# Optimization experiments

Measured on AMD Instinct MI355X. Metric: run time of the kernel, lower is better.

The kernel has to match this reference:

```python
import jax, jax.numpy as jnp
import numpy as np

N_NODES = 50000
N_EDGES = 400000
N_GRAPHS = 128
D_IN = 768
D_HID = 256
D_OUT = 256
EPS_COS = 1e-8
EPS_BN = 1e-5
NEG_SLOPE = 0.2  # PyG GATConv default


def setup_inputs() -> dict:
    key = jax.random.key(0)
    ks = jax.random.split(key, 16)
    inp = {
        "claim_emb": jax.random.normal(ks[0], (N_GRAPHS, D_IN), dtype=jnp.float32),
        "x": jax.random.normal(ks[1], (N_NODES, D_IN), dtype=jnp.float32),
        "edge_index": jax.random.randint(ks[2], (2, N_EDGES), 0, N_NODES, dtype=jnp.int64 if jax.config.jax_enable_x64 else jnp.int32),
        "node_batch": jnp.sort(jax.random.randint(ks[3], (N_NODES,), 0, N_GRAPHS, dtype=jnp.int64 if jax.config.jax_enable_x64 else jnp.int32)),
        # GAT layer 1 (768 -> 256, single head)
        "W1": jax.random.normal(ks[4], (D_IN, D_HID), dtype=jnp.float32) * (1.0 / np.sqrt(D_IN)),
        "a_src1": jax.random.normal(ks[5], (D_HID,), dtype=jnp.float32) * 0.1,
        "a_dst1": jax.random.normal(ks[6], (D_HID,), dtype=jnp.float32) * 0.1,
        "b1": jnp.zeros((D_HID,), dtype=jnp.float32),
        # GAT layer 2 (256 -> 256)
        "W2": jax.random.normal(ks[7], (D_HID, D_OUT), dtype=jnp.float32) * (1.0 / np.sqrt(D_HID)),
        "a_src2": jax.random.normal(ks[8], (D_OUT,), dtype=jnp.float32) * 0.1,
        "a_dst2": jax.random.normal(ks[9], (D_OUT,), dtype=jnp.float32) * 0.1,
        "b2": jnp.zeros((D_OUT,), dtype=jnp.float32),
        # BatchNorm after layer 1
        "bn_gamma": jnp.ones((D_HID,), dtype=jnp.float32),
        "bn_beta": jnp.zeros((D_HID,), dtype=jnp.float32),
        # classifier: (gnn_out + claim_dim) -> 1
        "clf_W": jax.random.normal(ks[10], (D_OUT + D_IN, 1), dtype=jnp.float32) * (1.0 / np.sqrt(D_OUT + D_IN)),
        "clf_b": jnp.zeros((1,), dtype=jnp.float32),
    }
    return inp


def _gat_conv(x, src, dst, n_nodes, W, a_src, a_dst, b):
    """PyG GATConv, heads=1, concat=True, self-loops already appended to src/dst."""
    h = x @ W                                  # [N, H]
    alpha_s = h @ a_src                        # [N]
    alpha_d = h @ a_dst                        # [N]
    e = jax.nn.leaky_relu(alpha_s[src] + alpha_d[dst], NEG_SLOPE)  # [E]
    # segment softmax over edges grouped by destination node
    m = jax.ops.segment_max(e, dst, num_segments=n_nodes)          # [N]
    ex = jnp.exp(e - m[dst])
    denom = jax.ops.segment_sum(ex, dst, num_segments=n_nodes)     # [N]
    attn = ex / denom[dst]                                         # [E]
    out = jax.ops.segment_sum(h[src] * attn[:, None], dst, num_segments=n_nodes)
    return out + b


def reference(claim_emb, x, edge_index, node_batch,
              W1, a_src1, a_dst1, b1, W2, a_src2, a_dst2, b2,
              bn_gamma, bn_beta, clf_W, clf_b):
    n_nodes = x.shape[0]
    n_graphs = claim_emb.shape[0]

    # relevance weighting: cosine similarity between claim (per node's graph) and node feature
    ce = claim_emb[node_batch]                                      # [N, 768]
    dot = jnp.sum(ce * x, axis=-1)
    norm = jnp.linalg.norm(ce, axis=-1) * jnp.linalg.norm(x, axis=-1)
    rel = dot / jnp.maximum(norm, EPS_COS)                          # [N]
    h = x * rel[:, None]

    # add self loops (PyG GATConv default)
    loops = jnp.arange(n_nodes, dtype=edge_index.dtype)
    src = jnp.concatenate([edge_index[0], loops])
    dst = jnp.concatenate([edge_index[1], loops])

    # layer 1: GAT -> BatchNorm (training-mode batch stats) -> ReLU
    h = _gat_conv(h, src, dst, n_nodes, W1, a_src1, a_dst1, b1)
    mu = jnp.mean(h, axis=0)
    var = jnp.var(h, axis=0)
    h = (h - mu) / jnp.sqrt(var + EPS_BN) * bn_gamma + bn_beta
    h = jax.nn.relu(h)

    # layer 2: GAT -> ReLU
    h = _gat_conv(h, src, dst, n_nodes, W2, a_src2, a_dst2, b2)
    h = jax.nn.relu(h)

    # global mean pool per graph
    sums = jax.ops.segment_sum(h, node_batch, num_segments=n_graphs)            # [B, 256]
    counts = jax.ops.segment_sum(jnp.ones((n_nodes,), h.dtype), node_batch, num_segments=n_graphs)
    pooled = sums / jnp.maximum(counts, 1.0)[:, None]

    combined = jnp.concatenate([pooled, claim_emb], axis=1)                     # [B, 256+768]
    out = combined @ clf_W + clf_b                                              # [B, 1]
    return out[:, 0]
```

## Files before the change

### kernel.cpp

```cpp
#include <hip/hip_runtime.h>
#include <hip/hip_bf16.h>

#define N_NODES  50000
#define N_EDGES  400000
#define E_TOT    450000
#define N_GRAPHS 128
#define D_IN     768
#define D_HID    256

typedef __hip_bfloat16 bf16;
typedef __attribute__((ext_vector_type(8))) short short8;
typedef __attribute__((ext_vector_type(4))) short short4v;
typedef __attribute__((ext_vector_type(4))) float f32x4;

__device__ __forceinline__ float b2f(bf16 v) { return __bfloat162float(v); }
__device__ __forceinline__ float us2f(unsigned short u) { return __uint_as_float((unsigned)u << 16); }
__device__ __forceinline__ int clampN(int v) { return min(max(v, 0), N_NODES - 1); }
__device__ __forceinline__ short f2bs(float f) {
  unsigned u = __float_as_uint(f);
  return (short)((u + 0x7FFFu + ((u >> 16) & 1u)) >> 16);
}

__device__ __forceinline__ void gload_lds16(const void* g, void* l) {
  __builtin_amdgcn_global_load_lds(
      (const __attribute__((address_space(1))) void*)g,
      (__attribute__((address_space(3))) void*)l, 16, 0, 0);
}

__device__ __forceinline__ float waveReduceSum(float v) {
#pragma unroll
  for (int o = 32; o > 0; o >>= 1) v += __shfl_down(v, o);
  return v;
}

__device__ __forceinline__ float blockReduce256(float v, volatile float* buf4) {
  int lane = threadIdx.x & 63, wid = threadIdx.x >> 6;
  v = waveReduceSum(v);
  if (lane == 0) buf4[wid] = v;
  __syncthreads();
  float s = buf4[0] + buf4[1] + buf4[2] + buf4[3];
  __syncthreads();
  return s;
}

__global__ __launch_bounds__(256) void detect_idx_kernel(
    const int* __restrict__ edge32, int* __restrict__ flagNZ) {
  if (threadIdx.x == 0) *flagNZ = 0;
  __syncthreads();
  int t = threadIdx.x;
  int nz = 0;
#pragma unroll
  for (int i = 0; i < 4; ++i) {
    int idx = 2 * (t + i * 256) + 1;
    if (edge32[idx] != 0) nz = 1;
  }
  if (nz) atomicOr(flagNZ, 1);
}

__global__ __launch_bounds__(256) void normalize_idx_kernel(
    const void* __restrict__ edge, const void* __restrict__ nbin,
    const int* __restrict__ flagNZ,
    int* __restrict__ src32, int* __restrict__ dst32, int* __restrict__ nb32,
    int* __restrict__ deg,
    const float* __restrict__ W1, const float* __restrict__ W2,
    short* __restrict__ W1T, short* __restrict__ W2T) {
  bool is64 = (*flagNZ == 0);
  long i = (long)blockIdx.x * 256 + threadIdx.x;
  const int*       e32 = (const int*)edge;
  const long long* e64 = (const long long*)edge;
  const int*       n32 = (const int*)nbin;
  const long long* n64 = (const long long*)nbin;
  if (i < N_NODES) deg[i] = 0;
  if (i < N_EDGES) {
    src32[i] = clampN(is64 ? (int)e64[i] : e32[i]);
    dst32[i] = clampN(is64 ? (int)e64[N_EDGES + i] : e32[N_EDGES + i]);
  }
  long j = i - N_EDGES;
  if (j >= 0 && j < N_NODES)
    nb32[j] = min(max(is64 ? (int)n64[j] : n32[j], 0), N_GRAPHS - 1);
  int t = (int)i;
  if (t < D_IN * D_HID) {
    int n = t / D_IN, k = t - n * D_IN;
    W1T[t] = f2bs(W1[(size_t)k * D_HID + n]);
  }
  int j2 = t - D_IN * D_HID;
  if (j2 >= 0 && j2 < D_HID * D_HID) {
    int n = j2 / D_HID, k = j2 - n * D_HID;
    W2T[j2] = f2bs(W2[(size_t)k * D_HID + n]);
  }
}

__global__ __launch_bounds__(256) void hist_kernel(
    const int* __restrict__ dst, int* __restrict__ deg) {
  int i = blockIdx.x * 256 + threadIdx.x;
  if (i >= E_TOT) return;
  int d = (i < N_EDGES) ? dst[i] : (i - N_EDGES);
  atomicAdd(&deg[d], 1);
}

#define SCAN_VPT 4
#define SCAN_BLK (256 * SCAN_VPT)
#define SCAN_NB  ((N_NODES + SCAN_BLK - 1) / SCAN_BLK)

__global__ __launch_bounds__(256) void scan_local_kernel(
    const int* __restrict__ deg, int* __restrict__ incl, int* __restrict__ blockSums) {
  __shared__ int wsum[4];
  int lane = threadIdx.x & 63, wid = threadIdx.x >> 6;
  int tbase = blockIdx.x * SCAN_BLK + threadIdx.x * SCAN_VPT;
  int v[SCAN_VPT];
  int s = 0;
#pragma unroll
  for (int j = 0; j < SCAN_VPT; ++j) {
    int i = tbase + j;
    v[j] = (i < N_NODES) ? deg[i] : 0;
    s += v[j];
  }
  int sc = s;
#pragma unroll
  for (int o = 1; o < 64; o <<= 1) {
    int t = __shfl_up(sc, o);
    if (lane >= o) sc += t;
  }
  if (lane == 63) wsum[wid] = sc;
  __syncthreads();
  int woff = 0;
  for (int w = 0; w < wid; ++w) woff += wsum[w];
  int run = woff + sc - s;
#pragma unroll
  for (int j = 0; j < SCAN_VPT; ++j) {
    run += v[j];
    int i = tbase + j;
    if (i < N_NODES) incl[i] = run;
  }
  if (threadIdx.x == 255)
    blockSums[blockIdx.x] = woff + sc;
}

__global__ __launch_bounds__(256) void scan_add_kernel(
    const int* __restrict__ deg, const int* __restrict__ incl,
    const int* __restrict__ bsums,
    int* __restrict__ rowptr, int* __restrict__ pos) {
  __shared__ int offSh;
  int sb = blockIdx.x >> 2;
  if (threadIdx.x < 64) {
    int v = (threadIdx.x < sb) ? bsums[threadIdx.x] : 0;
#pragma unroll
    for (int o = 32; o > 0; o >>= 1) v += __shfl_down(v, o);
    if (threadIdx.x == 0) offSh = v;
  }
  __syncthreads();
  int i = blockIdx.x * 256 + threadIdx.x;
  if (i >= N_NODES) return;
  int ic = incl[i] + offSh;
  rowptr[i + 1] = ic;
  pos[i] = ic - deg[i];
  if (i == 0) rowptr[0] = 0;
}

__global__ __launch_bounds__(256) void scatter_kernel(
    const int* __restrict__ src, const int* __restrict__ dst,
    int* __restrict__ pos, int* __restrict__ srcS) {
  int i = blockIdx.x * 256 + threadIdx.x;
  if (i >= E_TOT) return;
  int s, d;
  if (i < N_EDGES) { s = src[i]; d = dst[i]; } else { s = d = i - N_EDGES; }
  int j = atomicAdd(&pos[d], 1);
  srcS[j] = s;
}

__global__ __launch_bounds__(256) void rel_conv_kernel(
    const float* __restrict__ x, const float* __restrict__ claim,
    const int* __restrict__ nb, short* __restrict__ Abf,
    float* __restrict__ alphas, float* __restrict__ alphad,
    float* __restrict__ bnsums, float* __restrict__ bnsq) {
  int wid = threadIdx.x >> 6, lane = threadIdx.x & 63;
  int n = blockIdx.x * 4 + wid;
  if (blockIdx.x == 0) { bnsums[threadIdx.x] = 0.f; bnsq[threadIdx.x] = 0.f; }
  if (n >= N_NODES) return;
  if (lane == 0) { alphas[n] = 0.f; alphad[n] = 0.f; }
  int g = nb[n];
  const f32x4* xr = (const f32x4*)(x + (size_t)n * D_IN);
  const f32x4* cr = (const f32x4*)(claim + (size_t)g * D_IN);
  f32x4 xv[3];
  float dot = 0.f, nx = 0.f, nc = 0.f;
#pragma unroll
  for (int j = 0; j < 3; ++j) {
    xv[j] = xr[lane + j * 64];
    f32x4 cv = cr[lane + j * 64];
#pragma unroll
    for (int k = 0; k < 4; ++k) {
      dot += xv[j][k] * cv[k];
      nx  += xv[j][k] * xv[j][k];
      nc  += cv[k] * cv[k];
    }
  }
#pragma unroll
  for (int o = 32; o > 0; o >>= 1) {
    dot += __shfl_xor(dot, o);
    nx  += __shfl_xor(nx, o);
    nc  += __shfl_xor(nc, o);
  }
  float rel = dot / fmaxf(sqrtf(nx) * sqrtf(nc), 1e-8f);
  short4v* ab = (short4v*)(Abf + (size_t)n * D_IN);
#pragma unroll
  for (int j = 0; j < 3; ++j) {
    short4v o4;
#pragma unroll
    for (int k = 0; k < 4; ++k) o4[k] = f2bs(xv[j][k] * rel);
    ab[lane + j * 64] = o4;
  }
}

__global__ __launch_bounds__(256) void bn_conv_kernel(
    const float* __restrict__ agg, const float* __restrict__ sums,
    const float* __restrict__ sumsq, const float* __restrict__ gamma,
    const float* __restrict__ beta, short* __restrict__ A2,
    float* __restrict__ alphas, float* __restrict__ alphad,
    float* __restrict__ pooled) {
  int i = blockIdx.x * 256 + threadIdx.x;
  if ((i & 63) == 0) { int n = i >> 6; alphas[n] = 0.f; alphad[n] = 0.f; }
  if (i < N_GRAPHS * D_HID) pooled[i] = 0.f;
  f32x4 v = ((const f32x4*)agg)[i];
  int col = (i << 2) & (D_HID - 1);
  short4v o;
#pragma unroll
  for (int j = 0; j < 4; ++j) {
    float mu  = sums[col + j] * (1.f / N_NODES);
    float var = fmaxf(sumsq[col + j] * (1.f / N_NODES) - mu * mu, 0.f);
    float sc  = gamma[col + j] * rsqrtf(var + 1e-5f);
    float sh  = beta[col + j] - mu * sc;
    float t = fmaxf(v[j] * sc + sh, 0.f);
    o[j] = f2bs(t);
  }
  ((short4v*)A2)[i] = o;
}

#define GEMM_BK 32
__global__ __launch_bounds__(256) void mfma_gemm_bf16_kernel(
    const short* __restrict__ Abf, const short* __restrict__ BT,
    const float* __restrict__ aS, const float* __restrict__ aD,
    float* __restrict__ alphaS, float* __restrict__ alphaD,
    bf16* __restrict__ C, int M, int K) {
  __shared__ short As[4096];
  __shared__ short Bs[4096];
  int tid = threadIdx.x;
  int wave = tid >> 6, lane = tid & 63;
  int l16 = lane & 15, quadL = lane >> 4;
  int wr = wave >> 1, wc = wave & 1;
  int mBase = (blockIdx.x >> 1) * 128;
  int nBase = (blockIdx.x & 1) * 128;

  const short* gA[2];
  const short* gB[2];
  int ldsOff[2];
#pragma unroll
  for (int r = 0; r < 2; ++r) {
    int slot = r * 256 + tid;
    int mt = slot >> 6, quad = (slot >> 4) & 3, m16 = slot & 15;
    int rowA = min(mBase + mt * 16 + m16, M - 1);
    gA[r] = Abf + (size_t)rowA * K + quad * 8;
    gB[r] = BT + (size_t)(nBase + mt * 16 + m16) * K + quad * 8;
    ldsOff[r] = (r * 256 + wave * 64) * 8;
  }
  int aOff[4], bOff[4];
#pragma unroll
  for (int i = 0; i < 4; ++i) {
    aOff[i] = (wr * 4 + i) * 512 + quadL * 128 + l16 * 8;
    bOff[i] = (wc * 4 + i) * 512 + quadL * 128 + l16 * 8;
  }

  f32x4 acc[4][4] = {};

  for (int k0 = 0; k0 < K; k0 += GEMM_BK) {
#pragma unroll
    for (int r = 0; r < 2; ++r) {
      gload_lds16(gA[r] + k0, As + ldsOff[r]);
      gload_lds16(gB[r] + k0, Bs + ldsOff[r]);
    }
    __syncthreads();
    short8 af[4], bfv[4];
#pragma unroll
    for (int i = 0; i < 4; ++i) af[i] = *(const short8*)(As + aOff[i]);
#pragma unroll
    for (int j = 0; j < 4; ++j) bfv[j] = *(const short8*)(Bs + bOff[j]);
#pragma unroll
    for (int i = 0; i < 4; ++i)
#pragma unroll
      for (int j = 0; j < 4; ++j)
        acc[i][j] = __builtin_amdgcn_mfma_f32_16x16x32_bf16(af[i], bfv[j], acc[i][j], 0, 0, 0);
    __syncthreads();
  }

  float asv[4], adv[4];
#pragma unroll
  for (int j = 0; j < 4; ++j) {
    int col = nBase + (wc * 4 + j) * 16 + l16;
    asv[j] = aS[col]; adv[j] = aD[col];
  }
#pragma unroll
  for (int i = 0; i < 4; ++i) {
    int m0 = mBase + (wr * 4 + i) * 16 + quadL * 4;
#pragma unroll
    for (int r = 0; r < 4; ++r) {
      int m = m0 + r;
      float ss = acc[i][0][r] * asv[0] + acc[i][1][r] * asv[1] +
                 acc[i][2][r] * asv[2] + acc[i][3][r] * asv[3];
      float dd = acc[i][0][r] * adv[0] + acc[i][1][r] * adv[1] +
                 acc[i][2][r] * adv[2] + acc[i][3][r] * adv[3];
#pragma unroll
      for (int o = 1; o < 16; o <<= 1) {
        ss += __shfl_xor(ss, o);
        dd += __shfl_xor(dd, o);
      }
      if (m < M) {
        if (l16 == 0) { atomicAdd(&alphaS[m], ss); atomicAdd(&alphaD[m], dd); }
#pragma unroll
        for (int j = 0; j < 4; ++j)
          C[(size_t)m * D_HID + nBase + (wc * 4 + j) * 16 + l16] =
              __float2bfloat16(acc[i][j][r]);
      }
    }
  }
}

__global__ __launch_bounds__(256) void gat_agg_kernel(
    const int* __restrict__ rowptr, const int* __restrict__ srcS,
    const float* __restrict__ as_, const float* __restrict__ ad_,
    const bf16* __restrict__ h, float* __restrict__ agg) {
  int wid = threadIdx.x >> 6, lane = threadIdx.x & 63;
  int n = blockIdx.x * 4 + wid;
  if (n >= N_NODES) return;
  int start = rowptr[n], end = rowptr[n + 1];
  int deg = end - start;
  float adn = ad_[n];
  int sidx = 0;
  float e0 = -1e30f;
  if (lane < deg) {
    sidx = srcS[start + lane];
    float e = as_[sidx] + adn;
    e0 = e > 0.f ? e : 0.2f * e;
  }
  float m = e0;
  for (int j0 = start + 64; j0 < end; j0 += 64) {
    int j = j0 + lane;
    if (j < end) {
      float e = as_[srcS[j]] + adn;
      e = e > 0.f ? e : 0.2f * e;
      m = fmaxf(m, e);
    }
  }
#pragma unroll
  for (int o = 32; o > 0; o >>= 1) m = fmaxf(m, __shfl_xor(m, o));
  float pw = (lane < deg) ? __expf(e0 - m) : 0.f;
  float ssum = pw;
  for (int j0 = start + 64; j0 < end; j0 += 64) {
    int j = j0 + lane;
    if (j < end) {
      float e = as_[srcS[j]] + adn;
      e = e > 0.f ? e : 0.2f * e;
      ssum += __expf(e - m);
    }
  }
#pragma unroll
  for (int o = 32; o > 0; o >>= 1) ssum += __shfl_xor(ssum, o);
  float a0 = 0.f, a1 = 0.f, a2 = 0.f, a3 = 0.f;
  const unsigned short* hp = (const unsigned short*)h;
  int c0 = min(deg, 64);
  for (int t = 0; t < c0; ++t) {
    int s = __shfl(sidx, t);
    float w = __shfl(pw, t);
    const ushort4 hv = *(const ushort4*)(hp + (size_t)s * D_HID + lane * 4);
    a0 += us2f(hv.x) * w;
    a1 += us2f(hv.y) * w;
    a2 += us2f(hv.z) * w;
    a3 += us2f(hv.w) * w;
  }
  for (int j = start + 64; j < end; ++j) {
    int s = srcS[j];
    float e = as_[s] + adn;
    e = e > 0.f ? e : 0.2f * e;
    float w = __expf(e - m);
    const ushort4 hv = *(const ushort4*)(hp + (size_t)s * D_HID + lane * 4);
    a0 += us2f(hv.x) * w;
    a1 += us2f(hv.y) * w;
    a2 += us2f(hv.z) * w;
    a3 += us2f(hv.w) * w;
  }
  float inv = 1.f / ssum;
  float4 o4 = {a0 * inv, a1 * inv, a2 * inv, a3 * inv};
  *(float4*)(agg + (size_t)n * D_HID + lane * 4) = o4;
}

__global__ __launch_bounds__(256) void bn_stats_kernel(
    const float* __restrict__ h, float* __restrict__ sums, float* __restrict__ sumsq) {
  int col = threadIdx.x;
  float s = 0.f, q = 0.f;
  for (int r = blockIdx.x; r < N_NODES; r += gridDim.x) {
    float v = h[(size_t)r * D_HID + col];
    s += v; q += v * v;
  }
  atomicAdd(&sums[col], s);
  atomicAdd(&sumsq[col], q);
}

__global__ __launch_bounds__(256) void pool_kernel(
    const float* __restrict__ h, const float* __restrict__ bias2,
    const int* __restrict__ nb, float* __restrict__ pooled) {
  int col = threadIdx.x;
  float bias = bias2[col];
  int chunk = (N_NODES + gridDim.x - 1) / gridDim.x;
  int r0 = blockIdx.x * chunk;
  int r1 = min(N_NODES, r0 + chunk);
  float acc = 0.f; int cur = -1;
  for (int r = r0; r < r1; ++r) {
    int g = nb[r];
    if (g != cur) {
      if (cur >= 0) atomicAdd(&pooled[(size_t)cur * D_HID + col], acc);
      acc = 0.f; cur = g;
    }
    acc += fmaxf(h[(size_t)r * D_HID + col] + bias, 0.f);
  }
  if (cur >= 0) atomicAdd(&pooled[(size_t)cur * D_HID + col], acc);
}

__global__ __launch_bounds__(256) void clf_kernel(
    const float* __restrict__ pooled, const int* __restrict__ nb,
    const float* __restrict__ claim, const float* __restrict__ clfW,
    const float* __restrict__ clfb, float* __restrict__ out) {
  __shared__ float buf[4];
  __shared__ int cntSh;
  int g = blockIdx.x;
  if (threadIdx.x == 0) {
    int lo = 0, hi = N_NODES;
    while (lo < hi) { int mid = (lo + hi) >> 1; if (nb[mid] < g) lo = mid + 1; else hi = mid; }
    int lb = lo; hi = N_NODES;
    while (lo < hi) { int mid = (lo + hi) >> 1; if (nb[mid] <= g) lo = mid + 1; else hi = mid; }
    cntSh = lo - lb;
  }
  __syncthreads();
  float inv = 1.f / fmaxf((float)cntSh, 1.f);
  float p = 0.f;
  for (int d = threadIdx.x; d < (D_HID + D_IN); d += 256) {
    float w = clfW[d];
    float v = (d < D_HID) ? pooled[(size_t)g * D_HID + d] * inv
                          : claim[(size_t)g * D_IN + (d - D_HID)];
    p += v * w;
  }
  p = blockReduce256(p, buf);
  if (threadIdx.x == 0) out[g] = p + clfb[0];
}

extern "C" void kernel_launch(void* const* d_in, const int* in_sizes, int n_in,
                              void* d_out, int out_size, void* d_ws, size_t ws_size,
                              hipStream_t stream) {
  const float* claim = (const float*)d_in[0];
  const float* x     = (const float*)d_in[1];
  const void*  edge  = d_in[2];
  const void*  nbin  = d_in[3];
  const float* W1    = (const float*)d_in[4];
  const float* as1   = (const float*)d_in[5];
  const float* ad1   = (const float*)d_in[6];
  const float* W2    = (const float*)d_in[8];
  const float* as2   = (const float*)d_in[9];
  const float* ad2   = (const float*)d_in[10];
  const float* b2v   = (const float*)d_in[11];
  const float* gamma = (const float*)d_in[12];
  const float* beta  = (const float*)d_in[13];
  const float* clfW  = (const float*)d_in[14];
  const float* clfb  = (const float*)d_in[15];
  float* out = (float*)d_out;

  char* wsb = (char*)d_ws;
  size_t off = 0;
  auto alloc = [&](size_t bytes) -> char* {
    char* p = wsb + off;
    off = (off + bytes + 255) & ~(size_t)255;
    return p;
  };
  int*   flagNZ = (int*)alloc(sizeof(int));
  int*   src32  = (int*)alloc((size_t)N_EDGES * sizeof(int));
  int*   dst32  = (int*)alloc((size_t)N_EDGES * sizeof(int));
  int*   nb32   = (int*)alloc((size_t)N_NODES * sizeof(int));
  int*   deg    = (int*)alloc((size_t)N_NODES * sizeof(int));
  int*   rowptr = (int*)alloc((size_t)(N_NODES + 1) * sizeof(int));
  int*   pos    = (int*)alloc((size_t)N_NODES * sizeof(int));
  int*   incl   = (int*)alloc((size_t)N_NODES * sizeof(int));
  int*   bsums  = (int*)alloc((size_t)SCAN_NB * sizeof(int));
  int*   srcS   = (int*)alloc((size_t)E_TOT * sizeof(int));
  short* W1T    = (short*)alloc((size_t)D_IN * D_HID * sizeof(short));
  short* W2T    = (short*)alloc((size_t)D_HID * D_HID * sizeof(short));
  float* alphas = (float*)alloc((size_t)N_NODES * sizeof(float));
  float* alphad = (float*)alloc((size_t)N_NODES * sizeof(float));
  float* bnsums = (float*)alloc(D_HID * sizeof(float));
  float* bnsq   = (float*)alloc(D_HID * sizeof(float));
  float* pooled = (float*)alloc((size_t)N_GRAPHS * D_HID * sizeof(float));
  float* agg    = (float*)alloc((size_t)N_NODES * D_HID * sizeof(float));
  bf16*  h      = (bf16*) alloc((size_t)N_NODES * D_HID * sizeof(bf16));
  short* Abf    = (short*)alloc((size_t)N_NODES * D_IN * sizeof(short));
  short* A2     = Abf;

  detect_idx_kernel<<<1, 256, 0, stream>>>((const int*)edge, flagNZ);
  normalize_idx_kernel<<<(N_EDGES + N_NODES + 255) / 256, 256, 0, stream>>>(
      edge, nbin, flagNZ, src32, dst32, nb32, deg, W1, W2, W1T, W2T);
  int egrid = (E_TOT + 255) / 256;
  hist_kernel<<<egrid, 256, 0, stream>>>(dst32, deg);
  scan_local_kernel<<<SCAN_NB, 256, 0, stream>>>(deg, incl, bsums);
  scan_add_kernel<<<(N_NODES + 255) / 256, 256, 0, stream>>>(deg, incl, bsums, rowptr, pos);
  scatter_kernel<<<egrid, 256, 0, stream>>>(src32, dst32, pos, srcS);

  int gemmGrid = ((N_NODES + 127) / 128) * 2;

  rel_conv_kernel<<<N_NODES / 4, 256, 0, stream>>>(
      x, claim, nb32, Abf, alphas, alphad, bnsums, bnsq);
  mfma_gemm_bf16_kernel<<<gemmGrid, 256, 0, stream>>>(
      Abf, W1T, as1, ad1, alphas, alphad, h, N_NODES, D_IN);
  gat_agg_kernel<<<N_NODES / 4, 256, 0, stream>>>(rowptr, srcS, alphas, alphad, h, agg);

  bn_stats_kernel<<<256, 256, 0, stream>>>(agg, bnsums, bnsq);

  bn_conv_kernel<<<(N_NODES * D_HID / 4 + 255) / 256, 256, 0, stream>>>(
      agg, bnsums, bnsq, gamma, beta, A2, alphas, alphad, pooled);
  mfma_gemm_bf16_kernel<<<gemmGrid, 256, 0, stream>>>(
      A2, W2T, as2, ad2, alphas, alphad, h, N_NODES, D_HID);
  gat_agg_kernel<<<N_NODES / 4, 256, 0, stream>>>(rowptr, srcS, alphas, alphad, h, agg);

  pool_kernel<<<256, 256, 0, stream>>>(agg, b2v, nb32, pooled);
  clf_kernel<<<N_GRAPHS, 256, 0, stream>>>(pooled, nb32, claim, clfW, clfb, out);
}
```

Measured before the change: 629.2 us.

## Fuse mean-pool into layer-2 aggregation and remap GEMM tiles and LDS layout

The separate pool kernel is removed. The layer-2 GAT aggregation now adds bias, applies ReLU and atomically accumulates each node's output into its graph's pooled row, so the 50000x256 float agg buffer is never written and re-read. The GEMM block index is remapped so that consecutive blocks cover both N halves of a group of 8 M tiles, which is meant to improve L2 reuse of A. The global-to-LDS load pattern and fragment offsets are also changed so each lane reads contiguous 16-byte chunks along K within a row. The fused pooling issues many float atomics onto only 128x256 addresses, which risks atomic contention.

```diff
diff --git a/kernel.cpp b/kernel.cpp
--- a/kernel.cpp
+++ b/kernel.cpp
@@ -247,8 +247,13 @@
   int wave = tid >> 6, lane = tid & 63;
   int l16 = lane & 15, quadL = lane >> 4;
   int wr = wave >> 1, wc = wave & 1;
-  int mBase = (blockIdx.x >> 1) * 128;
-  int nBase = (blockIdx.x & 1) * 128;
+  int B = blockIdx.x;
+  int p = (B >> 4) * 8 + (B & 7);
+  int q = (B >> 3) & 1;
+  int mTiles = (M + 127) >> 7;
+  if (p >= mTiles) return;
+  int mBase = p * 128;
+  int nBase = q * 128;
 
   const short* gA[2];
   const short* gB[2];
@@ -256,7 +261,7 @@
 #pragma unroll
   for (int r = 0; r < 2; ++r) {
     int slot = r * 256 + tid;
-    int mt = slot >> 6, quad = (slot >> 4) & 3, m16 = slot & 15;
+    int mt = slot >> 6, m16 = (slot >> 2) & 15, quad = slot & 3;
     int rowA = min(mBase + mt * 16 + m16, M - 1);
     gA[r] = Abf + (size_t)rowA * K + quad * 8;
     gB[r] = BT + (size_t)(nBase + mt * 16 + m16) * K + quad * 8;
@@ -265,8 +270,8 @@
   int aOff[4], bOff[4];
 #pragma unroll
   for (int i = 0; i < 4; ++i) {
-    aOff[i] = (wr * 4 + i) * 512 + quadL * 128 + l16 * 8;
-    bOff[i] = (wc * 4 + i) * 512 + quadL * 128 + l16 * 8;
+    aOff[i] = (wr * 4 + i) * 512 + l16 * 32 + quadL * 8;
+    bOff[i] = (wc * 4 + i) * 512 + l16 * 32 + quadL * 8;
   }
 
   f32x4 acc[4][4] = {};
@@ -323,10 +328,13 @@
   }
 }
 
+template <int FUSE_POOL>
 __global__ __launch_bounds__(256) void gat_agg_kernel(
     const int* __restrict__ rowptr, const int* __restrict__ srcS,
     const float* __restrict__ as_, const float* __restrict__ ad_,
-    const bf16* __restrict__ h, float* __restrict__ agg) {
+    const bf16* __restrict__ h, float* __restrict__ agg,
+    const int* __restrict__ nb, const float* __restrict__ bias2,
+    float* __restrict__ pooled) {
   int wid = threadIdx.x >> 6, lane = threadIdx.x & 63;
   int n = blockIdx.x * 4 + wid;
   if (n >= N_NODES) return;
@@ -387,8 +395,18 @@
     a3 += us2f(hv.w) * w;
   }
   float inv = 1.f / ssum;
-  float4 o4 = {a0 * inv, a1 * inv, a2 * inv, a3 * inv};
-  *(float4*)(agg + (size_t)n * D_HID + lane * 4) = o4;
+  if (FUSE_POOL) {
+    int g = nb[n];
+    const float* bb = bias2 + lane * 4;
+    float* pg = pooled + (size_t)g * D_HID + lane * 4;
+    atomicAdd(pg + 0, fmaxf(a0 * inv + bb[0], 0.f));
+    atomicAdd(pg + 1, fmaxf(a1 * inv + bb[1], 0.f));
+    atomicAdd(pg + 2, fmaxf(a2 * inv + bb[2], 0.f));
+    atomicAdd(pg + 3, fmaxf(a3 * inv + bb[3], 0.f));
+  } else {
+    float4 o4 = {a0 * inv, a1 * inv, a2 * inv, a3 * inv};
+    *(float4*)(agg + (size_t)n * D_HID + lane * 4) = o4;
+  }
 }
 
 __global__ __launch_bounds__(256) void bn_stats_kernel(
@@ -401,26 +419,6 @@
   }
   atomicAdd(&sums[col], s);
   atomicAdd(&sumsq[col], q);
-}
-
-__global__ __launch_bounds__(256) void pool_kernel(
-    const float* __restrict__ h, const float* __restrict__ bias2,
-    const int* __restrict__ nb, float* __restrict__ pooled) {
-  int col = threadIdx.x;
-  float bias = bias2[col];
-  int chunk = (N_NODES + gridDim.x - 1) / gridDim.x;
-  int r0 = blockIdx.x * chunk;
-  int r1 = min(N_NODES, r0 + chunk);
-  float acc = 0.f; int cur = -1;
-  for (int r = r0; r < r1; ++r) {
-    int g = nb[r];
-    if (g != cur) {
-      if (cur >= 0) atomicAdd(&pooled[(size_t)cur * D_HID + col], acc);
-      acc = 0.f; cur = g;
-    }
-    acc += fmaxf(h[(size_t)r * D_HID + col] + bias, 0.f);
-  }
-  if (cur >= 0) atomicAdd(&pooled[(size_t)cur * D_HID + col], acc);
 }
 
 __global__ __launch_bounds__(256) void clf_kernel(
@@ -508,13 +506,15 @@
   scan_add_kernel<<<(N_NODES + 255) / 256, 256, 0, stream>>>(deg, incl, bsums, rowptr, pos);
   scatter_kernel<<<egrid, 256, 0, stream>>>(src32, dst32, pos, srcS);
 
-  int gemmGrid = ((N_NODES + 127) / 128) * 2;
+  int mTiles = (N_NODES + 127) / 128;
+  int gemmGrid = ((mTiles + 7) / 8) * 16;
 
   rel_conv_kernel<<<N_NODES / 4, 256, 0, stream>>>(
       x, claim, nb32, Abf, alphas, alphad, bnsums, bnsq);
   mfma_gemm_bf16_kernel<<<gemmGrid, 256, 0, stream>>>(
       Abf, W1T, as1, ad1, alphas, alphad, h, N_NODES, D_IN);
-  gat_agg_kernel<<<N_NODES / 4, 256, 0, stream>>>(rowptr, srcS, alphas, alphad, h, agg);
+  gat_agg_kernel<0><<<N_NODES / 4, 256, 0, stream>>>(
+      rowptr, srcS, alphas, alphad, h, agg, nb32, b2v, pooled);
 
   bn_stats_kernel<<<256, 256, 0, stream>>>(agg, bnsums, bnsq);
 
@@ -522,8 +522,8 @@
       agg, bnsums, bnsq, gamma, beta, A2, alphas, alphad, pooled);
   mfma_gemm_bf16_kernel<<<gemmGrid, 256, 0, stream>>>(
       A2, W2T, as2, ad2, alphas, alphad, h, N_NODES, D_HID);
-  gat_agg_kernel<<<N_NODES / 4, 256, 0, stream>>>(rowptr, srcS, alphas, alphad, h, agg);
-
-  pool_kernel<<<256, 256, 0, stream>>>(agg, b2v, nb32, pooled);
+  gat_agg_kernel<1><<<N_NODES / 4, 256, 0, stream>>>(
+      rowptr, srcS, alphas, alphad, h, agg, nb32, b2v, pooled);
+
   clf_kernel<<<N_GRAPHS, 256, 0, stream>>>(pooled, nb32, claim, clfW, clfb, out);
 }
```

New measurement: 735.9 us. 17.0% more time.
